# Kernel optimization log

Measured on AMD Instinct MI355X. Metric: run time of the kernel, lower is better.

The kernel has to match this reference:

```python
import jax, jax.numpy as jnp
import numpy as np
from jax import lax

B, N, D, H, E, K = 16, 1024, 1024, 4096, 8, 2


def setup_inputs() -> dict:
    key = jax.random.key(0)
    ks = jax.random.split(key, 12)
    s = 0.02
    return {
        "x": jax.random.normal(ks[0], (B, N, D), jnp.float32),
        "alpha": jnp.asarray(0.9, jnp.float32),
        "w_gate": jax.random.normal(ks[1], (D, E), jnp.float32) * s,
        "b_gate": jnp.zeros((E,), jnp.float32),
        "W1m": jax.random.normal(ks[2], (D, H), jnp.float32) * s,
        "b1m": jnp.zeros((H,), jnp.float32),
        "W2m": jax.random.normal(ks[3], (H, D), jnp.float32) * s,
        "b2m": jnp.zeros((D,), jnp.float32),
        "W1e": jax.random.normal(ks[4], (E, D, H), jnp.float32) * s,
        "b1e": jnp.zeros((E, H), jnp.float32),
        "W2e": jax.random.normal(ks[5], (E, H, D), jnp.float32) * s,
        "b2e": jnp.zeros((E, D), jnp.float32),
    }


def reference(x, alpha, w_gate, b_gate, W1m, b1m, W2m, b2m, W1e, b1e, W2e, b2e):
    # ---- main path: FFN (B,N,D) -> (B,N,D) ----
    main = jax.nn.gelu(x @ W1m + b1m) @ W2m + b2m

    # ---- router: per-sample mean-pooled gate, softmax, top-k ----
    logits = jnp.mean(x, axis=1) @ w_gate + b_gate            # [B,E]
    probs = jax.nn.softmax(logits, axis=-1)
    top_vals, top_idx = lax.top_k(probs, K)                    # [B,K]
    gate_w = top_vals / jnp.sum(top_vals, axis=-1, keepdims=True)  # renormalized

    # ---- expert path: gather per-assignment expert weights, batched FFN ----
    W1g = W1e[top_idx]                                        # [B,K,D,H]
    b1g = b1e[top_idx]                                        # [B,K,H]
    W2g = W2e[top_idx]                                        # [B,K,H,D]
    b2g = b2e[top_idx]                                        # [B,K,D]
    h = jax.nn.gelu(jnp.einsum('bnd,bkdh->bknh', x, W1g) + b1g[:, :, None, :])
    eo = jnp.einsum('bknh,bkhd->bknd', h, W2g) + b2g[:, :, None, :]
    expert_out = jnp.einsum('bk,bknd->bnd', gate_w, eo)       # weighted combine

    # ---- alpha mixing: alpha*main + (1-alpha)*expert ----
    a = jnp.clip(alpha, 0.1, 1.0)
    return a * main + (1.0 - a) * expert_out
```

## Files before the change

### kernel.cpp

```cpp
#include <hip/hip_runtime.h>
#include <hip/hip_bf16.h>
#include <stddef.h>

typedef unsigned short ushort_t;
typedef __bf16 bf16x8 __attribute__((ext_vector_type(8)));
typedef float  f32x4  __attribute__((ext_vector_type(4)));

#define GAS __attribute__((address_space(1)))
#define LAS __attribute__((address_space(3)))

__device__ __forceinline__ ushort_t f2bf(float f) {
    union { float f; unsigned u; } v; v.f = f;
    unsigned r = v.u + 0x7fffu + ((v.u >> 16) & 1u);
    return (ushort_t)(r >> 16);
}

__device__ __forceinline__ float gelu_tanh(float x) {
    float u = 0.7978845608028654f * x * (1.0f + 0.044715f * x * x);
    float e = __builtin_amdgcn_exp2f(-2.8853900817779268f * u);
    return x * __builtin_amdgcn_rcpf(1.0f + e);
}

__device__ __forceinline__ void gload_lds16(const ushort_t* g, ushort_t* l) {
    __builtin_amdgcn_global_load_lds((const GAS void*)g, (LAS void*)l, 16, 0, 0);
}

__global__ __launch_bounds__(256) void k_convert_x_pool(const float* __restrict__ x,
                                                        ushort_t* __restrict__ Xbf,
                                                        float* __restrict__ part) {
    int b = blockIdx.x, c = blockIdx.y, t = threadIdx.x;
    int d = t * 4;
    const float* xp = x + ((size_t)b * 1024 + (size_t)c * 64) * 1024;
    ushort_t* op = Xbf + ((size_t)b * 1024 + (size_t)c * 64) * 1024;
    float s0 = 0, s1 = 0, s2 = 0, s3 = 0;
    for (int n = 0; n < 64; ++n) {
        float4 v = *(const float4*)(xp + (size_t)n * 1024 + d);
        s0 += v.x; s1 += v.y; s2 += v.z; s3 += v.w;
        ushort4 o; o.x = f2bf(v.x); o.y = f2bf(v.y); o.z = f2bf(v.z); o.w = f2bf(v.w);
        *(ushort4*)(op + (size_t)n * 1024 + d) = o;
    }
    float4 s; s.x = s0; s.y = s1; s.z = s2; s.w = s3;
    *(float4*)(part + ((size_t)b * 16 + c) * 1024 + d) = s;
}

__global__ __launch_bounds__(256) void k_router(const float* __restrict__ part,
                                                const float* __restrict__ w_gate,
                                                const float* __restrict__ b_gate,
                                                const float* __restrict__ alpha,
                                                int* __restrict__ eidx,
                                                float* __restrict__ gsw) {
    __shared__ float red[8 * 256];
    int b = blockIdx.x, t = threadIdx.x;
    float le[8];
#pragma unroll
    for (int e = 0; e < 8; ++e) le[e] = 0.f;
    for (int i = 0; i < 4; ++i) {
        int d = t + i * 256;
        float s = 0.f;
#pragma unroll
        for (int c = 0; c < 16; ++c) s += part[((size_t)b * 16 + c) * 1024 + d];
        s *= (1.0f / 1024.0f);
#pragma unroll
        for (int e = 0; e < 8; ++e) le[e] += s * w_gate[(size_t)d * 8 + e];
    }
#pragma unroll
    for (int e = 0; e < 8; ++e) red[e * 256 + t] = le[e];
    __syncthreads();
    for (int s2 = 128; s2 > 0; s2 >>= 1) {
        if (t < s2)
#pragma unroll
            for (int e = 0; e < 8; ++e) red[e * 256 + t] += red[e * 256 + t + s2];
        __syncthreads();
    }
    if (t == 0) {
        float lg[8];
#pragma unroll
        for (int e = 0; e < 8; ++e) lg[e] = red[e * 256] + b_gate[e];
        float mx = lg[0];
#pragma unroll
        for (int e = 1; e < 8; ++e) mx = fmaxf(mx, lg[e]);
        float pe[8];
#pragma unroll
        for (int e = 0; e < 8; ++e) pe[e] = expf(lg[e] - mx);
        int i0 = 0;
        for (int e = 1; e < 8; ++e) if (pe[e] > pe[i0]) i0 = e;
        int i1 = -1;
        for (int e = 0; e < 8; ++e) { if (e == i0) continue; if (i1 < 0 || pe[e] > pe[i1]) i1 = e; }
        float a = fminf(fmaxf(alpha[0], 0.1f), 1.0f);
        float inv = (1.0f - a) / (pe[i0] + pe[i1]);
        eidx[2 * b] = i0; eidx[2 * b + 1] = i1;
        gsw[2 * b] = pe[i0] * inv; gsw[2 * b + 1] = pe[i1] * inv;
    }
}

__global__ __launch_bounds__(256) void k_transpose_cvt(const float* __restrict__ src,
                                                       ushort_t* __restrict__ dst,
                                                       int R, int C) {
    __shared__ float tile[64][65];
    int z = blockIdx.z;
    const float* s = src + (size_t)z * R * C;
    ushort_t* d = dst + (size_t)z * R * C;
    int c0 = blockIdx.x * 64, r0 = blockIdx.y * 64;
    int t = threadIdx.x;
    int tc = (t & 15) * 4, tr = t >> 4;
#pragma unroll
    for (int i = 0; i < 4; ++i) {
        int r = tr + i * 16;
        float4 v = *(const float4*)(s + (size_t)(r0 + r) * C + c0 + tc);
        tile[r][tc] = v.x; tile[r][tc + 1] = v.y; tile[r][tc + 2] = v.z; tile[r][tc + 3] = v.w;
    }
    __syncthreads();
    int wc = t >> 2, wr = (t & 3) * 16;
#pragma unroll
    for (int i = 0; i < 4; ++i) {
        ushort4 o;
        o.x = f2bf(tile[wr + i * 4 + 0][wc]);
        o.y = f2bf(tile[wr + i * 4 + 1][wc]);
        o.z = f2bf(tile[wr + i * 4 + 2][wc]);
        o.w = f2bf(tile[wr + i * 4 + 3][wc]);
        *(ushort4*)(d + (size_t)(c0 + wc) * R + r0 + wr + i * 4) = o;
    }
}

template <int NSEG, typename Epi>
__device__ __forceinline__ void gemm128(const ushort_t* A0, const ushort_t* A1,
                                        const ushort_t* B0, const ushort_t* B1,
                                        int segK, int m0, int n0, Epi epi) {
    __shared__ ushort_t lA[128 * 64];
    __shared__ ushort_t lB[128 * 64];
    const int tid = threadIdx.x;
    const int lane = tid & 63;
    const int wave = tid >> 6;
    const int quad = lane >> 4;
    const int l15 = lane & 15;
    const int sw = l15 & 7;
    const int wm = wave >> 1, wn = wave & 1;

    const int srow = 32 * wave + (lane >> 3);
    const int skg = (lane & 7) ^ (lane >> 3);
    ushort_t* la = lA + (size_t)wave * 2048;
    ushort_t* lb = lB + (size_t)wave * 2048;

    f32x4 acc[4][4] = {};
    const int steps = segK >> 6;

#pragma unroll 1
    for (int seg = 0; seg < NSEG; ++seg) {
        const ushort_t* A = (NSEG == 2 && seg == 1) ? A1 : A0;
        const ushort_t* B = (NSEG == 2 && seg == 1) ? B1 : B0;
        const size_t ro = (size_t)8 * segK;
        const ushort_t* pa = A + (size_t)(m0 + srow) * segK + skg * 8;
        const ushort_t* pb = B + (size_t)(n0 + srow) * segK + skg * 8;
#pragma unroll 1
        for (int kt = 0; kt < steps; ++kt) {
            gload_lds16(pa,           la);
            gload_lds16(pa +     ro,  la +  512);
            gload_lds16(pa + 2 * ro,  la + 1024);
            gload_lds16(pa + 3 * ro,  la + 1536);
            gload_lds16(pb,           lb);
            gload_lds16(pb +     ro,  lb +  512);
            gload_lds16(pb + 2 * ro,  lb + 1024);
            gload_lds16(pb + 3 * ro,  lb + 1536);
            pa += 64; pb += 64;
            __syncthreads();
            const bf16x8* pAf = (const bf16x8*)lA;
            const bf16x8* pBf = (const bf16x8*)lB;
#pragma unroll
            for (int h = 0; h < 2; ++h) {
                bf16x8 af[4], bfr[4];
#pragma unroll
                for (int mi = 0; mi < 4; ++mi)
                    af[mi] = pAf[(wm * 64 + mi * 16 + l15) * 8 + ((h * 4 + quad) ^ sw)];
#pragma unroll
                for (int ni = 0; ni < 4; ++ni)
                    bfr[ni] = pBf[(wn * 64 + ni * 16 + l15) * 8 + ((h * 4 + quad) ^ sw)];
#pragma unroll
                for (int mi = 0; mi < 4; ++mi)
#pragma unroll
                    for (int ni = 0; ni < 4; ++ni)
                        acc[mi][ni] = __builtin_amdgcn_mfma_f32_16x16x32_bf16(af[mi], bfr[ni], acc[mi][ni], 0, 0, 0);
            }
            __syncthreads();
        }
    }
#pragma unroll
    for (int mi = 0; mi < 4; ++mi)
#pragma unroll
        for (int ni = 0; ni < 4; ++ni)
            epi(m0 + wm * 64 + mi * 16 + quad * 4, n0 + wn * 64 + ni * 16 + l15, acc[mi][ni]);
}

struct EpiGeluStore {
    ushort_t* H; int ldh; const float* bias; float scale;
    __device__ void operator()(int r, int c, f32x4 v) const {
        float bc = bias[c];
#pragma unroll
        for (int i = 0; i < 4; ++i)
            H[(size_t)(r + i) * ldh + c] = f2bf(scale * gelu_tanh(v[i] + bc));
    }
};
struct EpiMainOut {
    float* out; const float* bias; float a;
    __device__ void operator()(int r, int c, f32x4 v) const {
        float bc = bias[c];
#pragma unroll
        for (int i = 0; i < 4; ++i) out[(size_t)(r + i) * 1024 + c] = a * (v[i] + bc);
    }
};
struct EpiExpertOut {
    float* out; const float* b0; const float* b1; float g0, g1;
    __device__ void operator()(int r, int c, f32x4 v) const {
        float bc = g0 * b0[c] + g1 * b1[c];
#pragma unroll
        for (int i = 0; i < 4; ++i) out[(size_t)(r + i) * 1024 + c] += v[i] + bc;
    }
};


__global__ __launch_bounds__(256) void k_gemm_main1(const ushort_t* __restrict__ Xbf,
                                                    const ushort_t* __restrict__ W1mT,
                                                    const float* __restrict__ b1m,
                                                    ushort_t* __restrict__ Hm) {
    int id = blockIdx.x, xcd = id & 7, slot = id >> 3;
    int g = slot >> 6;
    int u = slot & 63;
    int tm = xcd * 16 + (g & 1) * 8 + (u & 7);
    int tn = (g >> 1) * 8 + (u >> 3);
    EpiGeluStore epi{Hm, 4096, b1m, 1.0f};
    gemm128<1>(Xbf, Xbf, W1mT, W1mT, 1024, tm * 128, tn * 128, epi);
}
__global__ __launch_bounds__(256) void k_gemm_main2(const ushort_t* __restrict__ Hm,
                                                    const ushort_t* __restrict__ W2mT,
                                                    const float* __restrict__ b2m,
                                                    const float* __restrict__ alpha,
                                                    float* __restrict__ out) {
    int id = blockIdx.x, xcd = id & 7, slot = id >> 3;
    int g = slot >> 5;
    int u = slot & 31;
    int tm = xcd * 16 + g * 4 + (u & 3);
    int tn = u >> 2;
    float a = fminf(fmaxf(alpha[0], 0.1f), 1.0f);
    EpiMainOut epi{out, b2m, a};
    gemm128<1>(Hm, Hm, W2mT, W2mT, 4096, tm * 128, tn * 128, epi);
}
__global__ __launch_bounds__(256) void k_gemm_exp1(const ushort_t* __restrict__ Xbf,
                                                   const ushort_t* __restrict__ W1eT,
                                                   const float* __restrict__ b1e,
                                                   const int* __restrict__ eidx,
                                                   const float* __restrict__ gsw,
                                                   ushort_t* __restrict__ He) {
    int id = blockIdx.x, xcd = id & 7, slot = id >> 3;
    int j = xcd + 8 * (slot >> 8);
    int u2 = slot & 255;
    int g = u2 >> 6;
    int u = u2 & 63;
    int tm = u & 7;
    int tn = g * 8 + (u >> 3);
    int b = j >> 1;
    int e = eidx[j];
    float gs = gsw[j];
    const ushort_t* A = Xbf + (size_t)b * 1024 * 1024;
    const ushort_t* Bm = W1eT + (size_t)e * 4096 * 1024;
    EpiGeluStore epi{He + (size_t)j * 1024 * 4096, 4096, b1e + (size_t)e * 4096, gs};
    gemm128<1>(A, A, Bm, Bm, 1024, tm * 128, tn * 128, epi);
}
__global__ __launch_bounds__(256) void k_gemm_exp2(const ushort_t* __restrict__ He,
                                                   const ushort_t* __restrict__ W2eT,
                                                   const float* __restrict__ b2e,
                                                   const int* __restrict__ eidx,
                                                   const float* __restrict__ gsw,
                                                   float* __restrict__ out) {
    int id = blockIdx.x, xcd = id & 7, slot = id >> 3;
    int b = xcd + 8 * (slot >> 6);
    int tile = slot & 63;
    int tm = tile >> 3, tn = tile & 7;
    int e0 = eidx[2 * b], e1 = eidx[2 * b + 1];
    EpiExpertOut epi{out + (size_t)b * 1024 * 1024,
                     b2e + (size_t)e0 * 1024, b2e + (size_t)e1 * 1024,
                     gsw[2 * b], gsw[2 * b + 1]};
    gemm128<2>(He + (size_t)(2 * b) * 1024 * 4096, He + (size_t)(2 * b + 1) * 1024 * 4096,
               W2eT + (size_t)e0 * 1024 * 4096, W2eT + (size_t)e1 * 1024 * 4096,
               4096, tm * 128, tn * 128, epi);
}

extern "C" void kernel_launch(void* const* d_in, const int* in_sizes, int n_in,
                              void* d_out, int out_size, void* d_ws, size_t ws_size,
                              hipStream_t stream) {
    const float* x      = (const float*)d_in[0];
    const float* alpha  = (const float*)d_in[1];
    const float* w_gate = (const float*)d_in[2];
    const float* b_gate = (const float*)d_in[3];
    const float* W1m    = (const float*)d_in[4];
    const float* b1m    = (const float*)d_in[5];
    const float* W2m    = (const float*)d_in[6];
    const float* b2m    = (const float*)d_in[7];
    const float* W1e    = (const float*)d_in[8];
    const float* b1e    = (const float*)d_in[9];
    const float* W2e    = (const float*)d_in[10];
    const float* b2e    = (const float*)d_in[11];
    float* out = (float*)d_out;

    char* ws = (char*)d_ws;
    size_t off = 0;
    ushort_t* Xbf  = (ushort_t*)(ws + off); off += (size_t)16384 * 1024 * 2;
    ushort_t* W1mT = (ushort_t*)(ws + off); off += (size_t)4096 * 1024 * 2;
    ushort_t* W2mT = (ushort_t*)(ws + off); off += (size_t)4096 * 1024 * 2;
    ushort_t* W1eT = (ushort_t*)(ws + off); off += (size_t)8 * 4096 * 1024 * 2;
    ushort_t* W2eT = (ushort_t*)(ws + off); off += (size_t)8 * 4096 * 1024 * 2;
    float*    part = (float*)(ws + off);    off += (size_t)16 * 16 * 1024 * 4;
    int*      eidx = (int*)(ws + off);      off += 256;
    float*    gsw  = (float*)(ws + off);    off += 256;
    ushort_t* He   = (ushort_t*)(ws + off);
    ushort_t* Hm   = He;
    off += (size_t)32 * 1024 * 4096 * 2;
    if (ws_size < off) return;

    k_convert_x_pool<<<dim3(16, 16), 256, 0, stream>>>(x, Xbf, part);
    k_router<<<16, 256, 0, stream>>>(part, w_gate, b_gate, alpha, eidx, gsw);
    k_transpose_cvt<<<dim3(64, 16, 1), 256, 0, stream>>>(W1m, W1mT, 1024, 4096);
    k_transpose_cvt<<<dim3(16, 64, 1), 256, 0, stream>>>(W2m, W2mT, 4096, 1024);
    k_transpose_cvt<<<dim3(64, 16, 8), 256, 0, stream>>>(W1e, W1eT, 1024, 4096);
    k_transpose_cvt<<<dim3(16, 64, 8), 256, 0, stream>>>(W2e, W2eT, 4096, 1024);
    k_gemm_main1<<<4096, 256, 0, stream>>>(Xbf, W1mT, b1m, Hm);
    k_gemm_main2<<<1024, 256, 0, stream>>>(Hm, W2mT, b2m, alpha, out);
    k_gemm_exp1<<<8192, 256, 0, stream>>>(Xbf, W1eT, b1e, eidx, gsw, He);
    k_gemm_exp2<<<1024, 256, 0, stream>>>(He, W2eT, b2e, eidx, gsw, out);
}
```

Measured before the change: 1.535 ms.

## Replace 128x128 GEMM core with 256x256 triple-buffered pipelined tile

```diff
diff --git a/kernel.cpp b/kernel.cpp
--- a/kernel.cpp
+++ b/kernel.cpp
@@ -122,74 +122,6 @@
     }
 }
 
-template <int NSEG, typename Epi>
-__device__ __forceinline__ void gemm128(const ushort_t* A0, const ushort_t* A1,
-                                        const ushort_t* B0, const ushort_t* B1,
-                                        int segK, int m0, int n0, Epi epi) {
-    __shared__ ushort_t lA[128 * 64];
-    __shared__ ushort_t lB[128 * 64];
-    const int tid = threadIdx.x;
-    const int lane = tid & 63;
-    const int wave = tid >> 6;
-    const int quad = lane >> 4;
-    const int l15 = lane & 15;
-    const int sw = l15 & 7;
-    const int wm = wave >> 1, wn = wave & 1;
-
-    const int srow = 32 * wave + (lane >> 3);
-    const int skg = (lane & 7) ^ (lane >> 3);
-    ushort_t* la = lA + (size_t)wave * 2048;
-    ushort_t* lb = lB + (size_t)wave * 2048;
-
-    f32x4 acc[4][4] = {};
-    const int steps = segK >> 6;
-
-#pragma unroll 1
-    for (int seg = 0; seg < NSEG; ++seg) {
-        const ushort_t* A = (NSEG == 2 && seg == 1) ? A1 : A0;
-        const ushort_t* B = (NSEG == 2 && seg == 1) ? B1 : B0;
-        const size_t ro = (size_t)8 * segK;
-        const ushort_t* pa = A + (size_t)(m0 + srow) * segK + skg * 8;
-        const ushort_t* pb = B + (size_t)(n0 + srow) * segK + skg * 8;
-#pragma unroll 1
-        for (int kt = 0; kt < steps; ++kt) {
-            gload_lds16(pa,           la);
-            gload_lds16(pa +     ro,  la +  512);
-            gload_lds16(pa + 2 * ro,  la + 1024);
-            gload_lds16(pa + 3 * ro,  la + 1536);
-            gload_lds16(pb,           lb);
-            gload_lds16(pb +     ro,  lb +  512);
-            gload_lds16(pb + 2 * ro,  lb + 1024);
-            gload_lds16(pb + 3 * ro,  lb + 1536);
-            pa += 64; pb += 64;
-            __syncthreads();
-            const bf16x8* pAf = (const bf16x8*)lA;
-            const bf16x8* pBf = (const bf16x8*)lB;
-#pragma unroll
-            for (int h = 0; h < 2; ++h) {
-                bf16x8 af[4], bfr[4];
-#pragma unroll
-                for (int mi = 0; mi < 4; ++mi)
-                    af[mi] = pAf[(wm * 64 + mi * 16 + l15) * 8 + ((h * 4 + quad) ^ sw)];
-#pragma unroll
-                for (int ni = 0; ni < 4; ++ni)
-                    bfr[ni] = pBf[(wn * 64 + ni * 16 + l15) * 8 + ((h * 4 + quad) ^ sw)];
-#pragma unroll
-                for (int mi = 0; mi < 4; ++mi)
-#pragma unroll
-                    for (int ni = 0; ni < 4; ++ni)
-                        acc[mi][ni] = __builtin_amdgcn_mfma_f32_16x16x32_bf16(af[mi], bfr[ni], acc[mi][ni], 0, 0, 0);
-            }
-            __syncthreads();
-        }
-    }
-#pragma unroll
-    for (int mi = 0; mi < 4; ++mi)
-#pragma unroll
-        for (int ni = 0; ni < 4; ++ni)
-            epi(m0 + wm * 64 + mi * 16 + quad * 4, n0 + wn * 64 + ni * 16 + l15, acc[mi][ni]);
-}
-
 struct EpiGeluStore {
     ushort_t* H; int ldh; const float* bias; float scale;
     __device__ void operator()(int r, int c, f32x4 v) const {
@@ -216,71 +148,174 @@
     }
 };
 
-
-__global__ __launch_bounds__(256) void k_gemm_main1(const ushort_t* __restrict__ Xbf,
-                                                    const ushort_t* __restrict__ W1mT,
-                                                    const float* __restrict__ b1m,
-                                                    ushort_t* __restrict__ Hm) {
-    int id = blockIdx.x, xcd = id & 7, slot = id >> 3;
-    int g = slot >> 6;
-    int u = slot & 63;
-    int tm = xcd * 16 + (g & 1) * 8 + (u & 7);
-    int tn = (g >> 1) * 8 + (u >> 3);
+template <int NSEG, typename Epi>
+__device__ __forceinline__ void gemm256(const ushort_t* __restrict__ A0,
+                                        const ushort_t* __restrict__ A1,
+                                        const ushort_t* __restrict__ B0,
+                                        const ushort_t* __restrict__ B1,
+                                        int segK, int m0, int n0, Epi epi) {
+    __shared__ ushort_t lds[3 * 16384];
+    const int tid  = threadIdx.x;
+    const int lane = tid & 63;
+    const int w    = tid >> 6;
+    const int wm   = w >> 2, wn = w & 3;
+    const int l15  = lane & 15, quad = lane >> 4;
+
+    const int rs = (w << 4) + (lane >> 2);
+    const int gs = (((lane & 3) ^ ((rs >> 1) & 3)) << 3);
+    const size_t soA0 = (size_t)(m0 + rs) * segK + gs;
+    const size_t soA1 = soA0 + (size_t)128 * segK;
+    const size_t soB0 = (size_t)(n0 + rs) * segK + gs;
+    const size_t soB1 = soB0 + (size_t)128 * segK;
+
+    const int ntSeg = segK >> 5;
+    const int NT = NSEG * ntSeg;
+
+    auto stA = [&](int kt, int bsel) {
+        const ushort_t* S = (NSEG == 2 && kt >= ntSeg) ? A1 : A0;
+        int ktl = (NSEG == 2 && kt >= ntSeg) ? kt - ntSeg : kt;
+        const ushort_t* s0 = S + ((size_t)ktl << 5);
+        ushort_t* d = lds + bsel * 16384 + (w << 9);
+        gload_lds16(s0 + soA0, d);
+        gload_lds16(s0 + soA1, d + 4096);
+    };
+    auto stB = [&](int kt, int bsel) {
+        const ushort_t* S = (NSEG == 2 && kt >= ntSeg) ? B1 : B0;
+        int ktl = (NSEG == 2 && kt >= ntSeg) ? kt - ntSeg : kt;
+        const ushort_t* s0 = S + ((size_t)ktl << 5);
+        ushort_t* d = lds + bsel * 16384 + 8192 + (w << 9);
+        gload_lds16(s0 + soB0, d);
+        gload_lds16(s0 + soB1, d + 4096);
+    };
+
+    int aoffs[8], boffs[4];
+#pragma unroll
+    for (int mi = 0; mi < 8; ++mi) {
+        int r = wm * 128 + mi * 16 + l15;
+        aoffs[mi] = (r << 5) + ((quad ^ ((r >> 1) & 3)) << 3);
+    }
+#pragma unroll
+    for (int ni = 0; ni < 4; ++ni) {
+        int r = wn * 64 + ni * 16 + l15;
+        boffs[ni] = (r << 5) + ((quad ^ ((r >> 1) & 3)) << 3);
+    }
+
+    f32x4 acc[8][4] = {};
+
+    stA(0, 0); stB(0, 0);
+    stA(1, 1); stB(1, 1);
+    asm volatile("s_waitcnt vmcnt(4)" ::: "memory");
+    __builtin_amdgcn_s_barrier();
+
+    int cur = 0, nx2 = 2;
+#pragma unroll 1
+    for (int kt = 0; kt < NT; ++kt) {
+        const ushort_t* LA = lds + cur * 16384;
+        const ushort_t* LB = LA + 8192;
+        const bool st = (kt + 2 < NT);
+
+        bf16x8 af[4], bfr[4];
+#pragma unroll
+        for (int i = 0; i < 4; ++i) af[i]  = *(const bf16x8*)(LA + aoffs[i]);
+#pragma unroll
+        for (int i = 0; i < 4; ++i) bfr[i] = *(const bf16x8*)(LB + boffs[i]);
+        if (st) stA(kt + 2, nx2);
+        __builtin_amdgcn_s_barrier();
+        __builtin_amdgcn_s_setprio(1);
+#pragma unroll
+        for (int mi = 0; mi < 4; ++mi)
+#pragma unroll
+            for (int ni = 0; ni < 4; ++ni)
+                acc[mi][ni] = __builtin_amdgcn_mfma_f32_16x16x32_bf16(af[mi], bfr[ni], acc[mi][ni], 0, 0, 0);
+        __builtin_amdgcn_s_setprio(0);
+        __builtin_amdgcn_s_barrier();
+
+        bf16x8 ag[4];
+#pragma unroll
+        for (int i = 0; i < 4; ++i) ag[i] = *(const bf16x8*)(LA + aoffs[4 + i]);
+        if (st) stB(kt + 2, nx2);
+        __builtin_amdgcn_s_barrier();
+        __builtin_amdgcn_s_setprio(1);
+#pragma unroll
+        for (int mi = 0; mi < 4; ++mi)
+#pragma unroll
+            for (int ni = 0; ni < 4; ++ni)
+                acc[4 + mi][ni] = __builtin_amdgcn_mfma_f32_16x16x32_bf16(ag[mi], bfr[ni], acc[4 + mi][ni], 0, 0, 0);
+        __builtin_amdgcn_s_setprio(0);
+
+        __builtin_amdgcn_sched_barrier(0);
+        if (st) asm volatile("s_waitcnt vmcnt(4)" ::: "memory");
+        else    asm volatile("s_waitcnt vmcnt(0)" ::: "memory");
+        __builtin_amdgcn_s_barrier();
+
+        cur = (cur == 2) ? 0 : cur + 1;
+        nx2 = (nx2 == 2) ? 0 : nx2 + 1;
+    }
+
+#pragma unroll
+    for (int mi = 0; mi < 8; ++mi)
+#pragma unroll
+        for (int ni = 0; ni < 4; ++ni)
+            epi(m0 + wm * 128 + mi * 16 + quad * 4, n0 + wn * 64 + ni * 16 + l15, acc[mi][ni]);
+}
+
+__global__ __launch_bounds__(512, 2) void k_gemm_main1(const ushort_t* __restrict__ Xbf,
+                                                       const ushort_t* __restrict__ W1mT,
+                                                       const float* __restrict__ b1m,
+                                                       ushort_t* __restrict__ Hm) {
+    int id = blockIdx.x, xcd = id & 7, s = id >> 3;
+    int tile = xcd * 128 + s;
+    int tm = tile >> 4, tn = tile & 15;
     EpiGeluStore epi{Hm, 4096, b1m, 1.0f};
-    gemm128<1>(Xbf, Xbf, W1mT, W1mT, 1024, tm * 128, tn * 128, epi);
-}
-__global__ __launch_bounds__(256) void k_gemm_main2(const ushort_t* __restrict__ Hm,
-                                                    const ushort_t* __restrict__ W2mT,
-                                                    const float* __restrict__ b2m,
-                                                    const float* __restrict__ alpha,
-                                                    float* __restrict__ out) {
-    int id = blockIdx.x, xcd = id & 7, slot = id >> 3;
-    int g = slot >> 5;
-    int u = slot & 31;
-    int tm = xcd * 16 + g * 4 + (u & 3);
-    int tn = u >> 2;
+    gemm256<1>(Xbf, Xbf, W1mT, W1mT, 1024, tm * 256, tn * 256, epi);
+}
+__global__ __launch_bounds__(512, 2) void k_gemm_main2(const ushort_t* __restrict__ Hm,
+                                                       const ushort_t* __restrict__ W2mT,
+                                                       const float* __restrict__ b2m,
+                                                       const float* __restrict__ alpha,
+                                                       float* __restrict__ out) {
+    int id = blockIdx.x, xcd = id & 7, s = id >> 3;
+    int tile = xcd * 32 + s;
+    int tm = tile >> 2, tn = tile & 3;
     float a = fminf(fmaxf(alpha[0], 0.1f), 1.0f);
     EpiMainOut epi{out, b2m, a};
-    gemm128<1>(Hm, Hm, W2mT, W2mT, 4096, tm * 128, tn * 128, epi);
-}
-__global__ __launch_bounds__(256) void k_gemm_exp1(const ushort_t* __restrict__ Xbf,
-                                                   const ushort_t* __restrict__ W1eT,
-                                                   const float* __restrict__ b1e,
-                                                   const int* __restrict__ eidx,
-                                                   const float* __restrict__ gsw,
-                                                   ushort_t* __restrict__ He) {
-    int id = blockIdx.x, xcd = id & 7, slot = id >> 3;
-    int j = xcd + 8 * (slot >> 8);
-    int u2 = slot & 255;
-    int g = u2 >> 6;
-    int u = u2 & 63;
-    int tm = u & 7;
-    int tn = g * 8 + (u >> 3);
+    gemm256<1>(Hm, Hm, W2mT, W2mT, 4096, tm * 256, tn * 256, epi);
+}
+__global__ __launch_bounds__(512, 2) void k_gemm_exp1(const ushort_t* __restrict__ Xbf,
+                                                      const ushort_t* __restrict__ W1eT,
+                                                      const float* __restrict__ b1e,
+                                                      const int* __restrict__ eidx,
+                                                      const float* __restrict__ gsw,
+                                                      ushort_t* __restrict__ He) {
+    int id = blockIdx.x, xcd = id & 7, s = id >> 3;
+    int j = xcd * 4 + (s >> 6);
+    int t = s & 63;
+    int tm = t >> 4, tn = t & 15;
     int b = j >> 1;
     int e = eidx[j];
     float gs = gsw[j];
     const ushort_t* A = Xbf + (size_t)b * 1024 * 1024;
     const ushort_t* Bm = W1eT + (size_t)e * 4096 * 1024;
     EpiGeluStore epi{He + (size_t)j * 1024 * 4096, 4096, b1e + (size_t)e * 4096, gs};
-    gemm128<1>(A, A, Bm, Bm, 1024, tm * 128, tn * 128, epi);
-}
-__global__ __launch_bounds__(256) void k_gemm_exp2(const ushort_t* __restrict__ He,
-                                                   const ushort_t* __restrict__ W2eT,
-                                                   const float* __restrict__ b2e,
-                                                   const int* __restrict__ eidx,
-                                                   const float* __restrict__ gsw,
-                                                   float* __restrict__ out) {
-    int id = blockIdx.x, xcd = id & 7, slot = id >> 3;
-    int b = xcd + 8 * (slot >> 6);
-    int tile = slot & 63;
-    int tm = tile >> 3, tn = tile & 7;
+    gemm256<1>(A, A, Bm, Bm, 1024, tm * 256, tn * 256, epi);
+}
+__global__ __launch_bounds__(512, 2) void k_gemm_exp2(const ushort_t* __restrict__ He,
+                                                      const ushort_t* __restrict__ W2eT,
+                                                      const float* __restrict__ b2e,
+                                                      const int* __restrict__ eidx,
+                                                      const float* __restrict__ gsw,
+                                                      float* __restrict__ out) {
+    int id = blockIdx.x, xcd = id & 7, s = id >> 3;
+    int b = xcd * 2 + (s >> 4);
+    int t = s & 15;
+    int tm = t >> 2, tn = t & 3;
     int e0 = eidx[2 * b], e1 = eidx[2 * b + 1];
     EpiExpertOut epi{out + (size_t)b * 1024 * 1024,
                      b2e + (size_t)e0 * 1024, b2e + (size_t)e1 * 1024,
                      gsw[2 * b], gsw[2 * b + 1]};
-    gemm128<2>(He + (size_t)(2 * b) * 1024 * 4096, He + (size_t)(2 * b + 1) * 1024 * 4096,
+    gemm256<2>(He + (size_t)(2 * b) * 1024 * 4096, He + (size_t)(2 * b + 1) * 1024 * 4096,
                W2eT + (size_t)e0 * 1024 * 4096, W2eT + (size_t)e1 * 1024 * 4096,
-               4096, tm * 128, tn * 128, epi);
+               4096, tm * 256, tn * 256, epi);
 }
 
 extern "C" void kernel_launch(void* const* d_in, const int* in_sizes, int n_in,
@@ -321,8 +356,8 @@
     k_transpose_cvt<<<dim3(16, 64, 1), 256, 0, stream>>>(W2m, W2mT, 4096, 1024);
     k_transpose_cvt<<<dim3(64, 16, 8), 256, 0, stream>>>(W1e, W1eT, 1024, 4096);
     k_transpose_cvt<<<dim3(16, 64, 8), 256, 0, stream>>>(W2e, W2eT, 4096, 1024);
-    k_gemm_main1<<<4096, 256, 0, stream>>>(Xbf, W1mT, b1m, Hm);
-    k_gemm_main2<<<1024, 256, 0, stream>>>(Hm, W2mT, b2m, alpha, out);
-    k_gemm_exp1<<<8192, 256, 0, stream>>>(Xbf, W1eT, b1e, eidx, gsw, He);
-    k_gemm_exp2<<<1024, 256, 0, stream>>>(He, W2eT, b2e, eidx, gsw, out);
-}
+    k_gemm_main1<<<1024, 512, 0, stream>>>(Xbf, W1mT, b1m, Hm);
+    k_gemm_main2<<<256, 512, 0, stream>>>(Hm, W2mT, b2m, alpha, out);
+    k_gemm_exp1<<<2048, 512, 0, stream>>>(Xbf, W1eT, b1e, eidx, gsw, He);
+    k_gemm_exp2<<<256, 512, 0, stream>>>(He, W2eT, b2e, eidx, gsw, out);
+}
```

Measured after the change: 1.266 ms. 17.6% less time.
